# Kernel tuning notes

Hardware: AMD Instinct MI355X
Metric: run time of the kernel (lower is better)

Reference implementation:

```python
import jax, jax.numpy as jnp
import numpy as np

S = 41          # seq_len
D_IN = 1280
D_OUT = 1024
HEADS = 4
HC = D_OUT // HEADS
EPS = 1e-5

# ---- static edge construction (faithful to the torch code, incl. duplicate edges) ----

def _local_edges(s, window=1):
    e = []
    for i in range(s):
        for j in range(max(0, i - window), min(s, i + window + 1)):
            if i != j:
                e += [(i, j), (j, i)]
    return np.array(e, dtype=np.int32).T

def _region_edges(s):
    e = []
    step = s // 3
    for st in range(0, s, step):
        blk = range(st, min(st + step, s))
        for i in blk:
            for j in blk:
                if i != j:
                    e += [(i, j), (j, i)]
    return np.array(e, dtype=np.int32).T

def _global_edges(s):
    r, c = np.triu_indices(s, 1)  # torch.combinations: (i, j) with i < j
    return np.stack([r, c]).astype(np.int32)

def _batch_edges(e, b, s):
    off = np.arange(b, dtype=np.int32) * s
    return (e[:, None, :] + off[None, :, None]).reshape(2, -1)

_LOCAL = _local_edges(S)
_REGION = _region_edges(S)
_GLOBAL = _global_edges(S)

# ---- layer primitives ----

def _layernorm(x, g, b):
    mu = x.mean(-1, keepdims=True)
    v = ((x - mu) ** 2).mean(-1, keepdims=True)
    return (x - mu) / jnp.sqrt(v + EPS) * g + b

def _gcn(x, w, b, src, tgt, n):
    # PyG GCNConv: x' = D^-1/2 (A + I) D^-1/2 (x W) + b
    h = x @ w
    sl = jnp.arange(n, dtype=src.dtype)
    s = jnp.concatenate([src, sl]); t = jnp.concatenate([tgt, sl])
    deg = jax.ops.segment_sum(jnp.ones(t.shape, h.dtype), t, n)
    dinv = jnp.where(deg > 0, jax.lax.rsqrt(jnp.maximum(deg, 1.0)), 0.0)
    norm = dinv[s] * dinv[t]
    return jax.ops.segment_sum(h[s] * norm[:, None], t, n) + b

def _gat(x, w, a_src, a_dst, b, src, tgt, n):
    # PyG GATConv (shared lin, self loops, leaky_relu 0.2, softmax over incoming edges)
    h = (x @ w).reshape(n, HEADS, HC)
    sl = jnp.arange(n, dtype=src.dtype)
    s = jnp.concatenate([src, sl]); t = jnp.concatenate([tgt, sl])
    al_s = (h * a_src).sum(-1)  # [n, H]
    al_d = (h * a_dst).sum(-1)
    e = jax.nn.leaky_relu(al_s[s] + al_d[t], 0.2)  # [E, H]
    m = jax.ops.segment_max(e, t, n)
    ex = jnp.exp(e - m[t])
    den = jax.ops.segment_sum(ex, t, n)
    alpha = ex / den[t]
    out = jax.ops.segment_sum(h[s] * alpha[:, :, None], t, n)
    return out.reshape(n, HEADS * HC) + b

def _sage(x, wl, bl, wr, src, tgt, n):
    # PyG SAGEConv: mean-aggregate neighbors, plus root transform
    cnt = jax.ops.segment_sum(jnp.ones(src.shape, x.dtype), tgt, n)
    agg = jax.ops.segment_sum(x[src], tgt, n) / jnp.maximum(cnt, 1.0)[:, None]
    return agg @ wl + bl + x @ wr


def setup_inputs() -> dict:
    key = jax.random.key(0)
    ks = jax.random.split(key, 16)
    sc = 0.02
    f32 = jnp.float32
    inp = {
        'x': jax.random.normal(ks[0], (512, S, D_IN), f32),
        'att_w': jax.random.normal(ks[1], (D_IN, 1), f32) * sc,
        'att_b': jnp.zeros((1,), f32),
        'gcn_w': jax.random.normal(ks[2], (D_IN, D_OUT), f32) * sc,
        'gcn_b': jnp.zeros((D_OUT,), f32),
        'sn_g': jnp.ones((D_OUT,), f32), 'sn_b': jnp.zeros((D_OUT,), f32),
        'gat_w': jax.random.normal(ks[3], (D_IN, D_OUT), f32) * sc,
        'gat_as': jax.random.normal(ks[4], (HEADS, HC), f32) * sc,
        'gat_ad': jax.random.normal(ks[5], (HEADS, HC), f32) * sc,
        'gat_b': jnp.zeros((D_OUT,), f32),
        'mn_g': jnp.ones((D_OUT,), f32), 'mn_b': jnp.zeros((D_OUT,), f32),
        'sage_wl': jax.random.normal(ks[6], (D_IN, D_OUT), f32) * sc,
        'sage_bl': jnp.zeros((D_OUT,), f32),
        'sage_wr': jax.random.normal(ks[7], (D_IN, D_OUT), f32) * sc,
        'fp_w1': jax.random.normal(ks[8], (D_IN, 512), f32) * sc,
        'fp_b1': jnp.zeros((512,), f32),
        'fp_w2': jax.random.normal(ks[9], (512, S), f32) * sc,
        'fp_b2': jnp.zeros((S,), f32),
        'dn_g': jnp.ones((D_OUT,), f32), 'dn_b': jnp.zeros((D_OUT,), f32),
        'gate_w': jax.random.normal(ks[10], (3 * D_OUT, 3), f32) * sc,
        'gate_b': jnp.zeros((3,), f32),
    }
    return inp


def reference(x, att_w, att_b, gcn_w, gcn_b, sn_g, sn_b, gat_w, gat_as, gat_ad, gat_b,
              mn_g, mn_b, sage_wl, sage_bl, sage_wr, fp_w1, fp_b1, fp_w2, fp_b2,
              dn_g, dn_b, gate_w, gate_b):
    B = x.shape[0]
    N = B * S
    le = jnp.asarray(_batch_edges(_LOCAL, B, S))
    re = jnp.asarray(_batch_edges(_REGION, B, S))
    ge = jnp.asarray(_batch_edges(_GLOBAL, B, S))

    xf = x.reshape(N, D_IN)
    # shallow: local gating -> GCN -> LN
    enhanced = xf * jax.nn.sigmoid(xf @ att_w + att_b)
    shallow = _gcn(enhanced, gcn_w, gcn_b, le[0], le[1], N)
    shallow = _layernorm(shallow.reshape(B, S, D_OUT), sn_g, sn_b)
    # medium: GAT over region blocks -> LN
    gat = _gat(xf, gat_w, gat_as[None], gat_ad[None], gat_b, re[0], re[1], N)
    gat = _layernorm(gat.reshape(B, S, D_OUT), mn_g, mn_b)
    # deep: learned propagation mixing, SAGE over global edges -> LN
    pw = jax.nn.softmax(jax.nn.relu(x @ fp_w1 + fp_b1) @ fp_w2 + fp_b2, axis=-1)  # [B,S,S]
    sage_in = jnp.einsum('bij,bjd->bid', pw, x).reshape(N, D_IN)
    sage = _sage(sage_in, sage_wl, sage_bl, sage_wr, ge[0], ge[1], N)
    sage = _layernorm(sage.reshape(B, S, D_OUT), dn_g, dn_b)
    # gated branch mixing
    combined = jnp.concatenate([shallow, gat, sage], axis=-1)
    gates = jax.nn.softmax(combined @ gate_w + gate_b, axis=-1)
    total = gates[..., 0:1] * shallow + gates[..., 1:2] * gat + gates[..., 2:3] * sage
    return (shallow, gat, total)
```

## Files before the change

### kernel.cpp

```cpp
#include <hip/hip_runtime.h>
#include <math.h>

static constexpr int S    = 41;
static constexpr int DIN  = 1280;
static constexpr int DOUT = 1024;
static constexpr int HEADS = 4;
static constexpr int HC   = 256;

typedef __attribute__((ext_vector_type(4))) float f32x4;
typedef __attribute__((ext_vector_type(8))) short short8;

__device__ __forceinline__ ushort f2bf(float f) {
  uint u = __float_as_uint(f);
  uint r = u + 0x7fffu + ((u >> 16) & 1u);
  return (ushort)(r >> 16);
}
__device__ __forceinline__ float bf2f(ushort u) {
  return __uint_as_float(((uint)u) << 16);
}

__device__ __forceinline__ void gload16(const ushort* g, ushort* l) {
  __builtin_amdgcn_global_load_lds((const __attribute__((address_space(1))) void*)g,
                                   (__attribute__((address_space(3))) void*)l, 16, 0, 0);
}


__device__ __forceinline__ float warpReduceSum(float v) {
#pragma unroll
  for (int off = 32; off; off >>= 1) v += __shfl_down(v, off);
  return v;
}

__device__ __forceinline__ void blockReduce6(float* v) {
  __shared__ float red6[6][4];
  int w = threadIdx.x >> 6, lane = threadIdx.x & 63;
#pragma unroll
  for (int r = 0; r < 6; ++r) v[r] = warpReduceSum(v[r]);
  __syncthreads();
  if (lane == 0) {
#pragma unroll
    for (int r = 0; r < 6; ++r) red6[r][w] = v[r];
  }
  __syncthreads();
#pragma unroll
  for (int r = 0; r < 6; ++r)
    v[r] = red6[r][0] + red6[r][1] + red6[r][2] + red6[r][3];
}

__device__ __forceinline__ void blockReduce3v(float* v) {
  __shared__ float red3[3][4];
  int w = threadIdx.x >> 6, lane = threadIdx.x & 63;
#pragma unroll
  for (int r = 0; r < 3; ++r) v[r] = warpReduceSum(v[r]);
  __syncthreads();
  if (lane == 0) {
#pragma unroll
    for (int r = 0; r < 3; ++r) red3[r][w] = v[r];
  }
  __syncthreads();
#pragma unroll
  for (int r = 0; r < 3; ++r)
    v[r] = red3[r][0] + red3[r][1] + red3[r][2] + red3[r][3];
}


__global__ __launch_bounds__(256) void cvtsig_kernel(
    const float4* __restrict__ x, const float* __restrict__ att_w,
    const float* __restrict__ att_b, ushort4* __restrict__ xb, float* __restrict__ sig)
{
  int row  = blockIdx.x * 4 + (threadIdx.x >> 6);
  int lane = threadIdx.x & 63;
  const float4* xr = x + (size_t)row * (DIN / 4);
  const float4* wr = (const float4*)att_w;
  ushort4* xo = xb + (size_t)row * (DIN / 4);
  float acc = 0.f;
#pragma unroll
  for (int k = 0; k < DIN / 4 / 64; ++k) {
    float4 a = xr[lane + k * 64];
    float4 w = wr[lane + k * 64];
    acc += a.x * w.x + a.y * w.y + a.z * w.z + a.w * w.w;
    ushort4 o;
    o.x = f2bf(a.x); o.y = f2bf(a.y); o.z = f2bf(a.z); o.w = f2bf(a.w);
    xo[lane + k * 64] = o;
  }
  acc = warpReduceSum(acc);
  if (lane == 0) sig[row] = 1.f / (1.f + expf(-(acc + att_b[0])));
}


__global__ __launch_bounds__(256) void wcvt_kernel(const float* __restrict__ W,
                                                   ushort* __restrict__ out,
                                                   int K, int N, int ostride, int koff) {
  __shared__ float t[32][33];
  int n0 = blockIdx.x * 32, k0 = blockIdx.y * 32;
  int tx = threadIdx.x & 31, ty = threadIdx.x >> 5;
#pragma unroll
  for (int r = 0; r < 4; ++r) {
    int k = ty + r * 8;
    t[k][tx] = W[(size_t)(k0 + k) * N + n0 + tx];
  }
  __syncthreads();
#pragma unroll
  for (int r = 0; r < 4; ++r) {
    int nn = ty + r * 8;
    out[(size_t)(n0 + nn) * ostride + koff + k0 + tx] = f2bf(t[tx][nn]);
  }
}

__global__ __launch_bounds__(256) void w2cvt_kernel(const float* __restrict__ w2,
                                                    ushort* __restrict__ wpw) {
  int idx = blockIdx.x * 256 + threadIdx.x;
  int n = idx >> 9, k = idx & 511;
  wpw[idx] = (n < S) ? f2bf(w2[(size_t)k * S + n]) : (ushort)0;
}


struct Epi {
  void* dst[5];
  const float* bias[5];
  int nend[5];
  int ld[5];
  int relu[5];
  const float* rs;
};

template<bool F32OUT>
__global__ __launch_bounds__(256) void gemm_bf16(
    const ushort* __restrict__ A, const ushort* __restrict__ Bt, int K, int nb, Epi e)
{
  __shared__ __align__(16) ushort As[3][128 * 32];
  __shared__ __align__(16) ushort Bs[3][128 * 32];

  const int bid = blockIdx.x;
  const int bm  = (bid / nb) * 128;
  const int bn  = (bid % nb) * 128;

  const int tid  = threadIdx.x;
  const int w    = tid >> 6;
  const int lane = tid & 63;
  const int l16  = lane & 15;
  const int l4   = lane >> 4;
  const int m0   = (w >> 1) * 64;
  const int n0   = (w & 1) * 64;
  const int srow = w * 32 + (lane >> 2);
  const int scol = (lane & 3) * 8;

  f32x4 acc[4][4];
#pragma unroll
  for (int i = 0; i < 4; ++i)
#pragma unroll
    for (int j = 0; j < 4; ++j) acc[i][j] = (f32x4)0.f;

  const ushort* pA0 = A  + (size_t)(bm + srow) * K + scol;
  const ushort* pA1 = A  + (size_t)(bm + srow + 16) * K + scol;
  const ushort* pB0 = Bt + (size_t)(bn + srow) * K + scol;
  const ushort* pB1 = Bt + (size_t)(bn + srow + 16) * K + scol;

  auto stage = [&](int buf, int kt) {
    gload16(pA0 + kt, &As[buf][w * 1024]);
    gload16(pA1 + kt, &As[buf][w * 1024 + 512]);
    gload16(pB0 + kt, &Bs[buf][w * 1024]);
    gload16(pB1 + kt, &Bs[buf][w * 1024 + 512]);
  };

  const int nsteps = K >> 5;
  stage(0, 0); stage(1, 32); stage(2, 64);

  for (int t = 0; t < nsteps; ++t) {
    if (t == 0)                asm volatile("s_waitcnt vmcnt(8)" ::: "memory");
    else if (t == nsteps - 1)  asm volatile("s_waitcnt vmcnt(0)" ::: "memory");
    else                       asm volatile("s_waitcnt vmcnt(4)" ::: "memory");
    __builtin_amdgcn_s_barrier();
    asm volatile("" ::: "memory");

    if (t >= 1 && t + 2 < nsteps) stage((t + 2) % 3, (t + 2) * 32);

    const int cur = t % 3;
    short8 a[4], b[4];
#pragma unroll
    for (int i = 0; i < 4; ++i)
      a[i] = *reinterpret_cast<const short8*>(&As[cur][(m0 + i * 16 + l16) * 32 + l4 * 8]);
#pragma unroll
    for (int j = 0; j < 4; ++j)
      b[j] = *reinterpret_cast<const short8*>(&Bs[cur][(n0 + j * 16 + l16) * 32 + l4 * 8]);
#pragma unroll
    for (int i = 0; i < 4; ++i)
#pragma unroll
      for (int j = 0; j < 4; ++j)
        acc[i][j] = __builtin_amdgcn_mfma_f32_16x16x32_bf16(a[i], b[j], acc[i][j], 0, 0, 0);
  }

  void* dstv; const float* bias; const float* rs = nullptr; int ldc, cb, relu;
  if (bn < e.nend[0])      { dstv = e.dst[0]; ldc = e.ld[0]; cb = bn;             bias = e.bias[0]; relu = e.relu[0]; rs = e.rs; }
  else if (bn < e.nend[1]) { dstv = e.dst[1]; ldc = e.ld[1]; cb = bn - e.nend[0]; bias = e.bias[1]; relu = e.relu[1]; }
  else if (bn < e.nend[2]) { dstv = e.dst[2]; ldc = e.ld[2]; cb = bn - e.nend[1]; bias = e.bias[2]; relu = e.relu[2]; }
  else if (bn < e.nend[3]) { dstv = e.dst[3]; ldc = e.ld[3]; cb = bn - e.nend[2]; bias = e.bias[3]; relu = e.relu[3]; }
  else                     { dstv = e.dst[4]; ldc = e.ld[4]; cb = bn - e.nend[3]; bias = e.bias[4]; relu = e.relu[4]; }

#pragma unroll
  for (int i = 0; i < 4; ++i) {
    int mbase = bm + m0 + i * 16 + l4 * 4;
    float rsv[4];
#pragma unroll
    for (int r = 0; r < 4; ++r) rsv[r] = rs ? rs[mbase + r] : 1.f;
#pragma unroll
    for (int j = 0; j < 4; ++j) {
      int col = cb + n0 + j * 16 + l16;
      float bv = bias ? bias[col] : 0.f;
#pragma unroll
      for (int r = 0; r < 4; ++r) {
        float t = acc[i][j][r] * rsv[r] + bv;
        if (relu) t = fmaxf(t, 0.f);
        if (F32OUT) ((float*)dstv)[(size_t)(mbase + r) * ldc + col] = t;
        else        ((ushort*)dstv)[(size_t)(mbase + r) * ldc + col] = f2bf(t);
      }
    }
  }
}


__global__ __launch_bounds__(256) void mix_kernel(
    const float* __restrict__ fp2, const float* __restrict__ fp_b2,
    const ushort* __restrict__ xr, const ushort* __restrict__ xl,
    const float* __restrict__ sage_bl, ushort* __restrict__ hbuf)
{
  int b  = blockIdx.y;
  int d0 = blockIdx.x * 256;
  int tid = threadIdx.x, wv = tid >> 6, lane = tid & 63;
  __shared__ float pws[S][S];
  __shared__ float cpw[S][S];

  for (int i = wv; i < S; i += 4) {
    float v = (lane < S) ? (fp2[(size_t)(b * S + i) * 128 + lane] + fp_b2[lane]) : -1e30f;
    float m = v;
#pragma unroll
    for (int off = 32; off; off >>= 1) m = fmaxf(m, __shfl_xor(m, off));
    float e = (lane < S) ? expf(v - m) : 0.f;
    float sum = e;
#pragma unroll
    for (int off = 32; off; off >>= 1) sum += __shfl_xor(sum, off);
    if (lane < S) pws[i][lane] = e / sum;
  }
  __syncthreads();

  if (tid < S) {
    float run = 0.f;
    for (int i = 0; i < S; ++i) {
      cpw[i][tid] = (i > 0) ? run / (float)i : 0.f;
      run += pws[i][tid];
    }
  }
  __syncthreads();

  float xrv[S], xlv[S];
  const ushort* xrp = xr + (size_t)(b * S) * DOUT + d0 + tid;
  const ushort* xlp = xl + (size_t)(b * S) * DOUT + d0 + tid;
#pragma unroll
  for (int j = 0; j < S; ++j) {
    xrv[j] = bf2f(xrp[(size_t)j * DOUT]);
    xlv[j] = bf2f(xlp[(size_t)j * DOUT]);
  }
  float bl = sage_bl[d0 + tid];
  ushort* op = hbuf + (size_t)(b * S) * DOUT + d0 + tid;
  for (int i = 0; i < S; ++i) {
    float acc = bl;
#pragma unroll
    for (int j = 0; j < S; ++j)
      acc += pws[i][j] * xrv[j] + cpw[i][j] * xlv[j];
    op[(size_t)i * DOUT] = f2bf(acc);
  }
}


__device__ __forceinline__ float dinv_local(int j) {
  return rsqrtf((j == 0 || j == S - 1) ? 3.f : 5.f);
}

__global__ __launch_bounds__(256) void tail_fused(
    const ushort* __restrict__ gcnh, const ushort* __restrict__ Cgat,
    const ushort* __restrict__ hbuf,
    const float* __restrict__ gcn_b, const float* __restrict__ sn_g, const float* __restrict__ sn_b,
    const float* __restrict__ gat_as, const float* __restrict__ gat_ad, const float* __restrict__ gat_b,
    const float* __restrict__ mn_g, const float* __restrict__ mn_b,
    const float* __restrict__ dn_g, const float* __restrict__ dn_b,
    const float* __restrict__ gw, const float* __restrict__ gb,
    float* __restrict__ out, int N)
{
  int b  = blockIdx.x >> 2;
  int rb = blockIdx.x & 3;
  int lo = rb * 13;
  int cnt = (rb < 3) ? 13 : 2;
  size_t OUT = (size_t)N * DOUT;
  int tid = threadIdx.x;
  int wv = tid >> 6, lane = tid & 63;
  int d0 = tid * 4;
  int head = tid >> 6;

  __shared__ __align__(16) ushort hs[13][DOUT];
  __shared__ float alpha[13][13][HEADS];
  __shared__ float als_l[13][HEADS], ald_l[13][HEADS];

  for (int r = 0; r < cnt; ++r) {
    const ushort4* src = (const ushort4*)(Cgat + (size_t)(b * S + lo + r) * DOUT);
    ((ushort4*)hs[r])[tid] = src[tid];
  }
  __syncthreads();

  {
    const float4* a4 = (const float4*)(gat_as + wv * HC);
    const float4* d4 = (const float4*)(gat_ad + wv * HC);
    float4 av = a4[lane], dv = d4[lane];
    for (int s = 0; s < cnt; ++s) {
      ushort4 hv4 = ((const ushort4*)&hs[s][wv * HC])[lane];
      float h0 = bf2f(hv4.x), h1 = bf2f(hv4.y), h2 = bf2f(hv4.z), h3 = bf2f(hv4.w);
      float a = h0 * av.x + h1 * av.y + h2 * av.z + h3 * av.w;
      float d = h0 * dv.x + h1 * dv.y + h2 * dv.z + h3 * dv.w;
      a = warpReduceSum(a);
      d = warpReduceSum(d);
      if (lane == 0) { als_l[s][wv] = a; ald_l[s][wv] = d; }
    }
  }
  __syncthreads();

  if (tid < cnt * HEADS) {
    int t = tid >> 2, hd = tid & 3;
    float myald = ald_l[t][hd];
    float m = -1e30f;
    for (int s = 0; s < cnt; ++s) {
      float v = als_l[s][hd] + myald;
      v = (v > 0.f) ? v : 0.2f * v;
      m = fmaxf(m, v);
    }
    float den = 0.f;
    for (int s = 0; s < cnt; ++s) {
      float v = als_l[s][hd] + myald;
      v = (v > 0.f) ? v : 0.2f * v;
      float ev = expf(v - m) * ((s == t) ? 1.f : 2.f);
      alpha[t][s][hd] = ev;
      den += ev;
    }
    float inv = 1.f / den;
    for (int s = 0; s < cnt; ++s) alpha[t][s][hd] *= inv;
  }
  __syncthreads();

  float4 gcnb4 = *(const float4*)(gcn_b + d0);
  float4 sng4  = *(const float4*)(sn_g + d0);
  float4 snb4  = *(const float4*)(sn_b + d0);
  float4 gatb4 = *(const float4*)(gat_b + d0);
  float4 mng4  = *(const float4*)(mn_g + d0);
  float4 mnb4  = *(const float4*)(mn_b + d0);
  float4 dng4  = *(const float4*)(dn_g + d0);
  float4 dnb4  = *(const float4*)(dn_b + d0);
  float gwsh[4][3], gwga[4][3], gwsa[4][3];
#pragma unroll
  for (int q = 0; q < 4; ++q)
#pragma unroll
    for (int c = 0; c < 3; ++c) {
      gwsh[q][c] = gw[(size_t)(d0 + q) * 3 + c];
      gwga[q][c] = gw[(size_t)(DOUT + d0 + q) * 3 + c];
      gwsa[q][c] = gw[(size_t)(2 * DOUT + d0 + q) * 3 + c];
    }

  for (int t = 0; t < cnt; ++t) {
    int i = lo + t;
    size_t n = (size_t)(b * S + i);

    float di = dinv_local(i);
    float wc = di * di;
    float wl = (i > 0)     ? 2.f * di * dinv_local(i - 1) : 0.f;
    float wr = (i < S - 1) ? 2.f * di * dinv_local(i + 1) : 0.f;
    const ushort* hc = gcnh + n * DOUT + d0;
    ushort4 c4  = *(const ushort4*)hc;
    ushort4 lft = (i > 0)     ? *(const ushort4*)(hc - DOUT) : ushort4{0, 0, 0, 0};
    ushort4 rgt = (i < S - 1) ? *(const ushort4*)(hc + DOUT) : ushort4{0, 0, 0, 0};
    const ushort* cp = (const ushort*)&c4;
    const ushort* lp = (const ushort*)&lft;
    const ushort* rp = (const ushort*)&rgt;
    const float* gbp = (const float*)&gcnb4;
    float sh[4];
#pragma unroll
    for (int q = 0; q < 4; ++q)
      sh[q] = wc * bf2f(cp[q]) + wl * bf2f(lp[q]) + wr * bf2f(rp[q]) + gbp[q];

    float ga[4] = {0.f, 0.f, 0.f, 0.f};
    for (int si = 0; si < cnt; ++si) {
      float aj = alpha[t][si][head];
      ushort4 hv = *(const ushort4*)&hs[si][d0];
      ga[0] += aj * bf2f(hv.x);
      ga[1] += aj * bf2f(hv.y);
      ga[2] += aj * bf2f(hv.z);
      ga[3] += aj * bf2f(hv.w);
    }
    const float* gab = (const float*)&gatb4;
#pragma unroll
    for (int q = 0; q < 4; ++q) ga[q] += gab[q];

    ushort4 s4v = *(const ushort4*)(hbuf + n * DOUT + d0);
    const ushort* sp = (const ushort*)&s4v;
    float sa[4];
#pragma unroll
    for (int q = 0; q < 4; ++q) sa[q] = bf2f(sp[q]);

    float red[6] = {0.f, 0.f, 0.f, 0.f, 0.f, 0.f};
#pragma unroll
    for (int q = 0; q < 4; ++q) {
      red[0] += sh[q]; red[1] += sh[q] * sh[q];
      red[2] += ga[q]; red[3] += ga[q] * ga[q];
      red[4] += sa[q]; red[5] += sa[q] * sa[q];
    }
    blockReduce6(red);
    float mu0 = red[0] * (1.f / DOUT), r0 = rsqrtf(red[1] * (1.f / DOUT) - mu0 * mu0 + 1e-5f);
    float mu1 = red[2] * (1.f / DOUT), r1 = rsqrtf(red[3] * (1.f / DOUT) - mu1 * mu1 + 1e-5f);
    float mu2 = red[4] * (1.f / DOUT), r2 = rsqrtf(red[5] * (1.f / DOUT) - mu2 * mu2 + 1e-5f);

    const float* sngp = (const float*)&sng4; const float* snbp = (const float*)&snb4;
    const float* mngp = (const float*)&mng4; const float* mnbp = (const float*)&mnb4;
    const float* dngp = (const float*)&dng4; const float* dnbp = (const float*)&dnb4;
    float shn[4], gan[4], san[4];
#pragma unroll
    for (int q = 0; q < 4; ++q) {
      shn[q] = (sh[q] - mu0) * r0 * sngp[q] + snbp[q];
      gan[q] = (ga[q] - mu1) * r1 * mngp[q] + mnbp[q];
      san[q] = (sa[q] - mu2) * r2 * dngp[q] + dnbp[q];
    }

    float p[3] = {0.f, 0.f, 0.f};
#pragma unroll
    for (int q = 0; q < 4; ++q) {
#pragma unroll
      for (int c = 0; c < 3; ++c)
        p[c] += shn[q] * gwsh[q][c] + gan[q] * gwga[q][c] + san[q] * gwsa[q][c];
    }
    blockReduce3v(p);
    float l0 = p[0] + gb[0], l1 = p[1] + gb[1], l2 = p[2] + gb[2];
    float m = fmaxf(l0, fmaxf(l1, l2));
    float e0 = expf(l0 - m), e1 = expf(l1 - m), e2 = expf(l2 - m);
    float inv = 1.f / (e0 + e1 + e2);
    float g0 = e0 * inv, g1 = e1 * inv, g2 = e2 * inv;

    float4 o0, o1, o2;
    float* o0p = (float*)&o0; float* o1p = (float*)&o1; float* o2p = (float*)&o2;
#pragma unroll
    for (int q = 0; q < 4; ++q) {
      o0p[q] = shn[q];
      o1p[q] = gan[q];
      o2p[q] = g0 * shn[q] + g1 * gan[q] + g2 * san[q];
    }
    *(float4*)(out + n * DOUT + d0)           = o0;
    *(float4*)(out + OUT + n * DOUT + d0)     = o1;
    *(float4*)(out + 2 * OUT + n * DOUT + d0) = o2;
  }
}


extern "C" void kernel_launch(void* const* d_in, const int* in_sizes, int n_in,
                              void* d_out, int out_size, void* d_ws, size_t ws_size,
                              hipStream_t stream) {
  const float* x       = (const float*)d_in[0];
  const float* att_w   = (const float*)d_in[1];
  const float* att_b   = (const float*)d_in[2];
  const float* gcn_w   = (const float*)d_in[3];
  const float* gcn_b   = (const float*)d_in[4];
  const float* sn_g    = (const float*)d_in[5];
  const float* sn_b    = (const float*)d_in[6];
  const float* gat_w   = (const float*)d_in[7];
  const float* gat_as  = (const float*)d_in[8];
  const float* gat_ad  = (const float*)d_in[9];
  const float* gat_b   = (const float*)d_in[10];
  const float* mn_g    = (const float*)d_in[11];
  const float* mn_b    = (const float*)d_in[12];
  const float* sage_wl = (const float*)d_in[13];
  const float* sage_bl = (const float*)d_in[14];
  const float* sage_wr = (const float*)d_in[15];
  const float* fp_w1   = (const float*)d_in[16];
  const float* fp_b1   = (const float*)d_in[17];
  const float* fp_w2   = (const float*)d_in[18];
  const float* fp_b2   = (const float*)d_in[19];
  const float* dn_g    = (const float*)d_in[20];
  const float* dn_b    = (const float*)d_in[21];
  const float* gate_w  = (const float*)d_in[22];
  const float* gate_b  = (const float*)d_in[23];

  const int B = in_sizes[0] / (S * DIN);
  const int N = B * S;
  const int MB = N / 128;
  const int NMEGA = 4608;
  float* out = (float*)d_out;

  char* ws = (char*)d_ws;
  size_t off = 0;
  auto alloc = [&](size_t bytes) { size_t p = off; off += (bytes + 255) & ~(size_t)255; return p; };
  ushort* xb   = (ushort*)(ws + alloc((size_t)N * DIN * 2));
  ushort* Bt   = (ushort*)(ws + alloc((size_t)NMEGA * DIN * 2));
  ushort* wpw  = (ushort*)(ws + alloc((size_t)128 * 512 * 2));
  ushort* gcnh = (ushort*)(ws + alloc((size_t)N * DOUT * 2));
  ushort* Cgat = (ushort*)(ws + alloc((size_t)N * DOUT * 2));
  ushort* xr   = (ushort*)(ws + alloc((size_t)N * DOUT * 2));
  ushort* xl   = (ushort*)(ws + alloc((size_t)N * DOUT * 2));
  ushort* hbuf = (ushort*)(ws + alloc((size_t)N * DOUT * 2));
  float*  fp2  = (float*)(ws + alloc((size_t)N * 128 * 4));
  float*  sig  = (float*)(ws + alloc((size_t)N * 4));
  ushort* fp1  = hbuf;

  dim3 blk(256);

  cvtsig_kernel<<<N / 4, blk, 0, stream>>>((const float4*)x, att_w, att_b, (ushort4*)xb, sig);
  wcvt_kernel<<<dim3(DOUT / 32, DIN / 32), blk, 0, stream>>>(gcn_w, Bt, DIN, DOUT, DIN, 0);
  wcvt_kernel<<<dim3(DOUT / 32, DIN / 32), blk, 0, stream>>>(gat_w, Bt + (size_t)1024 * DIN, DIN, DOUT, DIN, 0);
  wcvt_kernel<<<dim3(512 / 32, DIN / 32), blk, 0, stream>>>(fp_w1, Bt + (size_t)2048 * DIN, DIN, 512, DIN, 0);
  wcvt_kernel<<<dim3(DOUT / 32, DIN / 32), blk, 0, stream>>>(sage_wr, Bt + (size_t)2560 * DIN, DIN, DOUT, DIN, 0);
  wcvt_kernel<<<dim3(DOUT / 32, DIN / 32), blk, 0, stream>>>(sage_wl, Bt + (size_t)3584 * DIN, DIN, DOUT, DIN, 0);
  w2cvt_kernel<<<dim3(128 * 512 / 256), blk, 0, stream>>>(fp_w2, wpw);

  Epi e1;
  e1.dst[0] = gcnh; e1.dst[1] = Cgat; e1.dst[2] = fp1; e1.dst[3] = xr; e1.dst[4] = xl;
  e1.bias[0] = nullptr; e1.bias[1] = nullptr; e1.bias[2] = fp_b1; e1.bias[3] = nullptr; e1.bias[4] = nullptr;
  e1.nend[0] = 1024; e1.nend[1] = 2048; e1.nend[2] = 2560; e1.nend[3] = 3584; e1.nend[4] = 4608;
  e1.ld[0] = DOUT; e1.ld[1] = DOUT; e1.ld[2] = 512; e1.ld[3] = DOUT; e1.ld[4] = DOUT;
  e1.relu[0] = 0; e1.relu[1] = 0; e1.relu[2] = 1; e1.relu[3] = 0; e1.relu[4] = 0;
  e1.rs = sig;
  gemm_bf16<false><<<dim3(MB * (NMEGA / 128)), blk, 0, stream>>>(xb, Bt, DIN, NMEGA / 128, e1);

  Epi epw;
  epw.dst[0] = fp2; epw.dst[1] = nullptr; epw.dst[2] = nullptr; epw.dst[3] = nullptr; epw.dst[4] = nullptr;
  epw.bias[0] = nullptr; epw.bias[1] = nullptr; epw.bias[2] = nullptr; epw.bias[3] = nullptr; epw.bias[4] = nullptr;
  epw.nend[0] = 1 << 30; epw.nend[1] = 1 << 30; epw.nend[2] = 1 << 30; epw.nend[3] = 1 << 30; epw.nend[4] = 1 << 30;
  epw.ld[0] = 128; epw.ld[1] = 128; epw.ld[2] = 128; epw.ld[3] = 128; epw.ld[4] = 128;
  epw.relu[0] = 0; epw.relu[1] = 0; epw.relu[2] = 0; epw.relu[3] = 0; epw.relu[4] = 0;
  epw.rs = nullptr;
  gemm_bf16<true><<<dim3(MB), blk, 0, stream>>>(fp1, wpw, 512, 1, epw);

  mix_kernel<<<dim3(DOUT / 256, B), blk, 0, stream>>>(fp2, fp_b2, xr, xl, sage_bl, hbuf);

  tail_fused<<<B * 4, blk, 0, stream>>>(gcnh, Cgat, hbuf,
                                        gcn_b, sn_g, sn_b,
                                        gat_as, gat_ad, gat_b,
                                        mn_g, mn_b, dn_g, dn_b,
                                        gate_w, gate_b, out, N);
}
```

Before: 704.8 us.

## Split mix softmax prep into its own kernel and raise MFMA wave priority

The per-batch softmax and cumulative-mean weight computation moves out of the mix kernel into a separate pwprep kernel that runs once per batch instead of once per 256-column slice. The mix kernel then reads the weights from a global buffer as uniform scalar loads instead of from LDS. The GEMM inner loop also wraps its MFMA block in s_setprio to favour waves issuing matrix ops. The price is an extra kernel launch and a global round trip for the weight tables.

After: 677.6 us. 1.04x faster.

```diff
diff --git a/kernel.cpp b/kernel.cpp
--- a/kernel.cpp
+++ b/kernel.cpp
@@ -183,11 +183,13 @@
 #pragma unroll
     for (int j = 0; j < 4; ++j)
       b[j] = *reinterpret_cast<const short8*>(&Bs[cur][(n0 + j * 16 + l16) * 32 + l4 * 8]);
+    __builtin_amdgcn_s_setprio(1);
 #pragma unroll
     for (int i = 0; i < 4; ++i)
 #pragma unroll
       for (int j = 0; j < 4; ++j)
         acc[i][j] = __builtin_amdgcn_mfma_f32_16x16x32_bf16(a[i], b[j], acc[i][j], 0, 0, 0);
+    __builtin_amdgcn_s_setprio(0);
   }
 
   void* dstv; const float* bias; const float* rs = nullptr; int ldc, cb, relu;
@@ -219,38 +221,47 @@
 }
 
 
-__global__ __launch_bounds__(256) void mix_kernel(
+__global__ __launch_bounds__(256) void pwprep_kernel(
     const float* __restrict__ fp2, const float* __restrict__ fp_b2,
-    const ushort* __restrict__ xr, const ushort* __restrict__ xl,
-    const float* __restrict__ sage_bl, ushort* __restrict__ hbuf)
+    float* __restrict__ pc)
+{
+  int b = blockIdx.x;
+  int tid = threadIdx.x, wv = tid >> 6, lane = tid & 63;
+  __shared__ float pws[S][S];
+  for (int i = wv; i < S; i += 4) {
+    float v = (lane < S) ? (fp2[(size_t)(b * S + i) * 128 + lane] + fp_b2[lane]) : -1e30f;
+    float m = v;
+#pragma unroll
+    for (int off = 32; off; off >>= 1) m = fmaxf(m, __shfl_xor(m, off));
+    float e = (lane < S) ? expf(v - m) : 0.f;
+    float sum = e;
+#pragma unroll
+    for (int off = 32; off; off >>= 1) sum += __shfl_xor(sum, off);
+    if (lane < S) {
+      float p = e / sum;
+      pws[i][lane] = p;
+      pc[((size_t)b * S + i) * 128 + lane] = p;
+    }
+  }
+  __syncthreads();
+  if (tid < S) {
+    float run = 0.f;
+    for (int i = 0; i < S; ++i) {
+      pc[((size_t)b * S + i) * 128 + 64 + tid] = (i > 0) ? run / (float)i : 0.f;
+      run += pws[i][tid];
+    }
+  }
+}
+
+
+__global__ __launch_bounds__(256) void mixc_kernel(
+    const float* __restrict__ pc, const ushort* __restrict__ xr,
+    const ushort* __restrict__ xl, const float* __restrict__ sage_bl,
+    ushort* __restrict__ hbuf)
 {
   int b  = blockIdx.y;
   int d0 = blockIdx.x * 256;
-  int tid = threadIdx.x, wv = tid >> 6, lane = tid & 63;
-  __shared__ float pws[S][S];
-  __shared__ float cpw[S][S];
-
-  for (int i = wv; i < S; i += 4) {
-    float v = (lane < S) ? (fp2[(size_t)(b * S + i) * 128 + lane] + fp_b2[lane]) : -1e30f;
-    float m = v;
-#pragma unroll
-    for (int off = 32; off; off >>= 1) m = fmaxf(m, __shfl_xor(m, off));
-    float e = (lane < S) ? expf(v - m) : 0.f;
-    float sum = e;
-#pragma unroll
-    for (int off = 32; off; off >>= 1) sum += __shfl_xor(sum, off);
-    if (lane < S) pws[i][lane] = e / sum;
-  }
-  __syncthreads();
-
-  if (tid < S) {
-    float run = 0.f;
-    for (int i = 0; i < S; ++i) {
-      cpw[i][tid] = (i > 0) ? run / (float)i : 0.f;
-      run += pws[i][tid];
-    }
-  }
-  __syncthreads();
+  int tid = threadIdx.x;
 
   float xrv[S], xlv[S];
   const ushort* xrp = xr + (size_t)(b * S) * DOUT + d0 + tid;
@@ -262,11 +273,13 @@
   }
   float bl = sage_bl[d0 + tid];
   ushort* op = hbuf + (size_t)(b * S) * DOUT + d0 + tid;
+  const float* pcb = pc + (size_t)(b * S) * 128;
   for (int i = 0; i < S; ++i) {
+    const float* row = pcb + (size_t)i * 128;
     float acc = bl;
 #pragma unroll
     for (int j = 0; j < S; ++j)
-      acc += pws[i][j] * xrv[j] + cpw[i][j] * xlv[j];
+      acc += row[j] * xrv[j] + row[64 + j] * xlv[j];
     op[(size_t)i * DOUT] = f2bf(acc);
   }
 }
@@ -500,6 +513,7 @@
   ushort* xl   = (ushort*)(ws + alloc((size_t)N * DOUT * 2));
   ushort* hbuf = (ushort*)(ws + alloc((size_t)N * DOUT * 2));
   float*  fp2  = (float*)(ws + alloc((size_t)N * 128 * 4));
+  float*  pc   = (float*)(ws + alloc((size_t)N * 128 * 4));
   float*  sig  = (float*)(ws + alloc((size_t)N * 4));
   ushort* fp1  = hbuf;
 
@@ -531,7 +545,8 @@
   epw.rs = nullptr;
   gemm_bf16<true><<<dim3(MB), blk, 0, stream>>>(fp1, wpw, 512, 1, epw);
 
-  mix_kernel<<<dim3(DOUT / 256, B), blk, 0, stream>>>(fp2, fp_b2, xr, xl, sage_bl, hbuf);
+  pwprep_kernel<<<B, blk, 0, stream>>>(fp2, fp_b2, pc);
+  mixc_kernel<<<dim3(DOUT / 256, B), blk, 0, stream>>>(pc, xr, xl, sage_bl, hbuf);
 
   tail_fused<<<B * 4, blk, 0, stream>>>(gcnh, Cgat, hbuf,
                                         gcn_b, sn_g, sn_b,
```
